# Performance work log

Hardware: AMD Instinct MI355X
Metric: run time of the kernel (lower is better)

The kernel has to match this reference:

```python
import jax, jax.numpy as jnp
import numpy as np

D_MODEL = 512
N_HEADS = 8
DH = D_MODEL // N_HEADS            # 64
Q_PROJ = D_MODEL // 2              # 256
KV_PROJ = (2 * D_MODEL) // 3       # 341
ROPE_DIM = D_MODEL // 8            # 64 total rope dims
R = ROPE_DIM // N_HEADS            # 8 rope dims per head
THETA = 10000.0
EPS = 1e-5
B, S = 2, 2048


def layernorm(x, g, b):
    m = jnp.mean(x, axis=-1, keepdims=True)
    v = jnp.var(x, axis=-1, keepdims=True)
    return (x - m) * jax.lax.rsqrt(v + EPS) * g + b


def rope_cos_sin(seq_len, dtype):
    inv_freq = THETA ** (-jnp.arange(0, R, 2, dtype=jnp.float32) / R)   # (R/2,)
    ang = jnp.arange(seq_len, dtype=jnp.float32)[:, None] * inv_freq   # (S, R/2)
    cos = jnp.concatenate([jnp.cos(ang), jnp.cos(ang)], axis=-1)        # (S, R)
    sin = jnp.concatenate([jnp.sin(ang), jnp.sin(ang)], axis=-1)
    return cos.astype(dtype), sin.astype(dtype)


def apply_rope(x, cos, sin):
    # x: (B, H, S, R); neox-style half rotation
    x1, x2 = jnp.split(x, 2, axis=-1)
    rot = jnp.concatenate([-x2, x1], axis=-1)
    return x * cos + rot * sin


def setup_inputs() -> dict:
    key = jax.random.key(0)
    ks = jax.random.split(key, 9)
    p = lambda k, shape: 0.01 * jax.random.normal(k, shape, jnp.float32)
    return {
        "x": jax.random.normal(ks[0], (B, S, D_MODEL), jnp.float32),
        "W_dq": p(ks[1], (D_MODEL, Q_PROJ)),
        "W_uq": p(ks[2], (Q_PROJ, D_MODEL)),
        "W_qr": p(ks[3], (Q_PROJ, ROPE_DIM)),
        "W_dkv": p(ks[4], (D_MODEL, KV_PROJ)),
        "W_ukv": p(ks[5], (KV_PROJ, 2 * D_MODEL)),
        "W_kr": p(ks[6], (D_MODEL, ROPE_DIM)),
        "W_o": p(ks[7], (D_MODEL, D_MODEL)),
        "q_ln_g": jnp.ones((Q_PROJ,), jnp.float32),
        "q_ln_b": jnp.zeros((Q_PROJ,), jnp.float32),
        "kv_ln_g": jnp.ones((KV_PROJ,), jnp.float32),
        "kv_ln_b": jnp.zeros((KV_PROJ,), jnp.float32),
    }


def reference(x, W_dq, W_uq, W_qr, W_dkv, W_ukv, W_kr, W_o,
              q_ln_g, q_ln_b, kv_ln_g, kv_ln_b):
    b, s, d = x.shape
    # --- low-rank Q path ---
    cq = layernorm(x @ W_dq, q_ln_g, q_ln_b)                      # (B,S,Q_PROJ)
    Q = (cq @ W_uq).reshape(b, s, N_HEADS, DH).transpose(0, 2, 1, 3)
    Qr = (cq @ W_qr).reshape(b, s, N_HEADS, R).transpose(0, 2, 1, 3)
    cos, sin = rope_cos_sin(s, x.dtype)
    Qr = apply_rope(Qr, cos, sin)
    q = jnp.concatenate([Q, Qr], axis=-1)                          # (B,H,S,DH+R)
    # --- low-rank KV path ---
    ckv = layernorm(x @ W_dkv, kv_ln_g, kv_ln_b)                  # (B,S,KV_PROJ)
    KV = ckv @ W_ukv                                              # (B,S,2*D)
    K, V = KV[..., :D_MODEL], KV[..., D_MODEL:]
    K = K.reshape(b, s, N_HEADS, DH).transpose(0, 2, 1, 3)
    Kr = (x @ W_kr).reshape(b, s, N_HEADS, R).transpose(0, 2, 1, 3)
    Kr = apply_rope(Kr, cos, sin)
    k = jnp.concatenate([K, Kr], axis=-1)                          # (B,H,S,DH+R)
    v = V.reshape(b, s, N_HEADS, DH).transpose(0, 2, 1, 3)         # (B,H,S,DH)
    # --- causal SDPA ---
    scale = 1.0 / jnp.sqrt(jnp.asarray(DH + R, x.dtype))
    scores = jnp.einsum('bhqd,bhkd->bhqk', q, k) * scale           # (B,H,S,S)
    mask = jnp.tril(jnp.ones((s, s), dtype=bool))
    scores = jnp.where(mask, scores, jnp.finfo(scores.dtype).min)
    attn = jax.nn.softmax(scores, axis=-1)
    out = jnp.einsum('bhqk,bhkd->bhqd', attn, v)
    out = out.transpose(0, 2, 1, 3).reshape(b, s, d)
    return out @ W_o.T, ckv
```

## Files before the change

### kernel.cpp

```cpp
#include <hip/hip_runtime.h>
#include <hip/hip_bf16.h>

#define BATCH 2
#define SEQ 2048
#define DM 512
#define NH 8
#define DHD 64
#define QP 256
#define KVP 341
#define DQKPAD 96
#define MROWS 4096

#define OFF_X     0
#define OFF_WO    2932224
#define OFF_QG    3194368
#define OFF_QB    3194624
#define OFF_KG    3194880
#define OFF_KB    3195221

#define T_DQ   0
#define T_DKV  131072
#define T_KR   327680
#define T_UQ   360448
#define T_QR   491520
#define T_UKV  507904
#define T_TOT  901120

#define NW_X   2097152
#define NW_WO  262144
#define NW_PAR 1194
#define PREP_TOT (NW_X + NW_WO + NW_PAR + T_TOT)

typedef __bf16 bf16x8 __attribute__((ext_vector_type(8)));
typedef float f32x4 __attribute__((ext_vector_type(4)));
typedef __hip_bfloat16 bf16;
typedef unsigned short u16;

static __device__ __forceinline__ bf16x8 ld_bf8(const bf16* p) {
    return __builtin_bit_cast(bf16x8, *(const uint4*)p);
}

#define GL16(gp, lp) __builtin_amdgcn_global_load_lds( \
    (const __attribute__((address_space(1))) void*)(gp), \
    (__attribute__((address_space(3))) void*)(lp), 16, 0, 0)

__global__ __launch_bounds__(256) void prep(
    const void* px, const void* pwdq, const void* pwuq, const void* pwqr,
    const void* pwdkv, const void* pwukv, const void* pwkr, const void* pwo,
    const void* pqg, const void* pqb, const void* pkg, const void* pkb,
    u16* __restrict__ arena, u16* __restrict__ WT, int* __restrict__ flagp)
{
    __shared__ int cnt;
    if (threadIdx.x == 0) cnt = 0;
    __syncthreads();
    int bad = 0;
    const u16* xs = (const u16*)px;
    for (int i = threadIdx.x; i < 2048; i += 256) {
        u16 u = xs[i];
        int e = (u >> 7) & 0xFF;
        if (u != 0 && (e < 90 || e > 164)) bad++;
    }
    #pragma unroll
    for (int m2 = 1; m2 < 64; m2 <<= 1) bad += __shfl_xor(bad, m2);
    if ((threadIdx.x & 63) == 0) atomicAdd(&cnt, bad);
    __syncthreads();
    const int f = (cnt > 256) ? 1 : 0;
    if (blockIdx.x == 0 && threadIdx.x == 0) *flagp = f;

    int gid = blockIdx.x * 256 + threadIdx.x;
    if (gid >= PREP_TOT) return;

    auto rdu = [&](const void* s, int i) -> u16 {
        if (f) return __builtin_bit_cast(u16, __float2bfloat16(((const float*)s)[i]));
        return ((const u16*)s)[i];
    };

    if (gid < NW_X) {
        arena[OFF_X + gid] = rdu(px, gid);
    } else if (gid < NW_X + NW_WO) {
        int i = gid - NW_X;
        arena[OFF_WO + i] = rdu(pwo, i);
    } else if (gid < NW_X + NW_WO + NW_PAR) {
        int i = gid - NW_X - NW_WO;
        if (i < 256)      arena[OFF_QG + i]         = rdu(pqg, i);
        else if (i < 512) arena[OFF_QB + (i - 256)] = rdu(pqb, i - 256);
        else if (i < 853) arena[OFF_KG + (i - 512)] = rdu(pkg, i - 512);
        else              arena[OFF_KB + (i - 853)] = rdu(pkb, i - 853);
    } else {
        int loc = gid - (NW_X + NW_WO + NW_PAR);
        const void* src; int srcIdx, valid;
        if (loc < T_DKV)      { int l2 = loc;          int n = l2 >> 9, k = l2 & 511; src = pwdq;  valid = 1;         srcIdx = k * 256 + n; }
        else if (loc < T_KR)  { int l2 = loc - T_DKV;  int n = l2 >> 9, k = l2 & 511; src = pwdkv; valid = (n < 341); srcIdx = k * 341 + n; }
        else if (loc < T_UQ)  { int l2 = loc - T_KR;   int n = l2 >> 9, k = l2 & 511; src = pwkr;  valid = 1;         srcIdx = k * 64 + n; }
        else if (loc < T_QR)  { int l2 = loc - T_UQ;   int n = l2 >> 8, k = l2 & 255; src = pwuq;  valid = 1;         srcIdx = k * 512 + n; }
        else if (loc < T_UKV) { int l2 = loc - T_QR;   int n = l2 >> 8, k = l2 & 255; src = pwqr;  valid = 1;         srcIdx = k * 64 + n; }
        else                  { int l2 = loc - T_UKV;  int n = l2 / 384, k = l2 % 384; src = pwukv; valid = (k < 341); srcIdx = k * 1024 + n; }
        WT[loc] = valid ? rdu(src, srcIdx) : (u16)0;
    }
}

static __device__ __forceinline__ void rope_epi(
    f32x4 (&acc)[2][4], bf16* __restrict__ dst, int m0, int w, int g, int lr, int tid, bool scaleq)
{
    const float SCv = 0.11785113019775793f;
    #pragma unroll
    for (int mt = 0; mt < 2; ++mt)
    #pragma unroll
    for (int r = 0; r < 4; ++r) {
        int gm = m0 + w * 32 + mt * 16 + g * 4 + r;
        int s = gm & 2047, b = gm >> 11;
        float ang = (float)s * exp2f(-(float)(lr & 3) * 3.3219280948873623f);
        float sn, cs;
        sincosf(ang, &sn, &cs);
        #pragma unroll
        for (int nt = 0; nt < 4; ++nt) {
            float v = acc[mt][nt][r];
            float pt = __shfl_xor(v, 4);
            float o = (lr & 4) ? fmaf(pt, sn, v * cs) : fmaf(-pt, sn, v * cs);
            if (scaleq) o *= SCv;
            int h = (nt * 16 + lr) >> 3, j = lr & 7;
            dst[((size_t)(b * NH + h) * SEQ + s) * DQKPAD + 64 + j] = __float2bfloat16(o);
        }
    }
    for (int u = tid; u < 128 * 96; u += 256) {
        int rw = u / 96, rem = u - rw * 96;
        int h = rem / 12, c = rem - h * 12;
        int row = m0 + rw, b2 = row >> 11, s2 = row & 2047;
        *(unsigned int*)&dst[((size_t)(b2 * NH + h) * SEQ + s2) * DQKPAD + 72 + c * 2] = 0u;
    }
}

__global__ __launch_bounds__(256) void gemm128(
    const bf16* __restrict__ A, int lda,
    const bf16* __restrict__ BT, int ldb,
    int N, int Kpad, int mode,
    void* __restrict__ C0, int ldc,
    bf16* __restrict__ kv_k, bf16* __restrict__ kv_v,
    const int* __restrict__ flagp, float* __restrict__ C0f)
{
    __shared__ __align__(16) bf16 LB[128 * 64 + 64 * 64];
    bf16* Al = LB;
    bf16* Bl = LB + 128 * 64;
    const int tid = threadIdx.x;
    const int m0 = blockIdx.y * 128, n0 = blockIdx.x * 64;
    const int lane = tid & 63, w = tid >> 6;
    const int g = lane >> 4, lr = lane & 15;
    f32x4 acc[2][4] = {};
    const int r8 = lane >> 3;
    const int xr8 = ((lane & 7) ^ r8) * 8;
    const int swx = (lr & 7) << 4;

    for (int k0 = 0; k0 < Kpad; k0 += 64) {
        #pragma unroll
        for (int i = 0; i < 4; ++i)
            GL16(&A[(size_t)(m0 + w * 32 + i * 8 + r8) * lda + k0 + xr8],
                 (char*)Al + w * 4096 + i * 1024);
        #pragma unroll
        for (int i = 0; i < 2; ++i)
            GL16(&BT[(size_t)(n0 + w * 16 + i * 8 + r8) * ldb + k0 + xr8],
                 (char*)Bl + w * 2048 + i * 1024);
        __syncthreads();
        #pragma unroll
        for (int ks = 0; ks < 2; ++ks) {
            const int cs = (ks * 64 + g * 16) ^ swx;
            bf16x8 a0 = ld_bf8((const bf16*)((const char*)Al + (w * 32 + lr) * 128 + cs));
            bf16x8 a1 = ld_bf8((const bf16*)((const char*)Al + (w * 32 + 16 + lr) * 128 + cs));
            #pragma unroll
            for (int nt = 0; nt < 4; ++nt) {
                bf16x8 b = ld_bf8((const bf16*)((const char*)Bl + (nt * 16 + lr) * 128 + cs));
                acc[0][nt] = __builtin_amdgcn_mfma_f32_16x16x32_bf16(a0, b, acc[0][nt], 0, 0, 0);
                acc[1][nt] = __builtin_amdgcn_mfma_f32_16x16x32_bf16(a1, b, acc[1][nt], 0, 0, 0);
            }
        }
        __syncthreads();
    }

    if (mode == 0 && n0 == 640) {
        rope_epi(acc, kv_k, m0, w, g, lr, tid, false);
        return;
    }
    if (mode == 4 && n0 == DM) {
        rope_epi(acc, (bf16*)C0, m0, w, g, lr, tid, true);
        return;
    }
    if (mode == 3 && n0 >= DM) {
        const int h = (n0 - DM) >> 6;
        const int b = m0 >> 11, s0 = m0 & 2047;
        bf16* T = LB;
        #pragma unroll
        for (int mt = 0; mt < 2; ++mt)
        #pragma unroll
        for (int nt = 0; nt < 4; ++nt)
        #pragma unroll
        for (int r = 0; r < 4; ++r) {
            int dv = nt * 16 + lr;
            int sl = w * 32 + mt * 16 + g * 4 + r;
            T[dv * 136 + sl] = __float2bfloat16(acc[mt][nt][r]);
        }
        __syncthreads();
        const int row = tid >> 2, coff = (tid & 3) * 32;
        bf16* dst = &kv_v[((size_t)(b * NH + h) * DHD + row) * SEQ + s0 + coff];
        const bf16* srcp = &T[row * 136 + coff];
        #pragma unroll
        for (int q2 = 0; q2 < 4; ++q2)
            *(uint4*)(dst + q2 * 8) = *(const uint4*)(srcp + q2 * 8);
        return;
    }

    const float SCv = 0.11785113019775793f;
    const int f32o = (mode == 1 && flagp) ? *flagp : 0;
    #pragma unroll
    for (int mt = 0; mt < 2; ++mt)
    #pragma unroll
    for (int nt = 0; nt < 4; ++nt)
    #pragma unroll
    for (int r = 0; r < 4; ++r) {
        int gm = m0 + w * 32 + mt * 16 + g * 4 + r;
        int gn = n0 + nt * 16 + lr;
        float v = acc[mt][nt][r];
        if (mode == 0) {
            ((float*)C0)[(size_t)gm * ldc + gn] = v;
        } else if (mode == 1) {
            if (f32o) C0f[(size_t)gm * ldc + gn] = v;
            else ((bf16*)C0)[(size_t)gm * ldc + gn] = __float2bfloat16(v);
        } else if (mode == 4) {
            int b = gm >> 11, s = gm & 2047;
            int h = gn >> 6, dh = gn & 63;
            ((bf16*)C0)[((size_t)(b * NH + h) * SEQ + s) * DQKPAD + dh] = __float2bfloat16(v * SCv);
        } else {
            int b = gm >> 11, s = gm & 2047;
            int h = gn >> 6, dh = gn & 63;
            kv_k[((size_t)(b * NH + h) * SEQ + s) * DQKPAD + dh] = __float2bfloat16(v);
        }
    }
}

__global__ __launch_bounds__(256) void ln_both(
    const float* __restrict__ y,
    const bf16* __restrict__ qg, const bf16* __restrict__ qb,
    const bf16* __restrict__ kg, const bf16* __restrict__ kb,
    bf16* __restrict__ cq, bf16* __restrict__ ckv_b, float* __restrict__ ckv_f,
    bf16* __restrict__ ckvp, const int* __restrict__ flagp)
{
    const int w = threadIdx.x >> 6, lane = threadIdx.x & 63;
    const int blk = blockIdx.x;
    if (blk < 1024) {
        const int row = blk * 4 + w;
        const float* yr = y + (size_t)row * 704;
        float s = 0.f, ss = 0.f;
        for (int i = lane; i < 256; i += 64) { float v = yr[i]; s += v; ss += v * v; }
        #pragma unroll
        for (int m = 1; m < 64; m <<= 1) { s += __shfl_xor(s, m); ss += __shfl_xor(ss, m); }
        float mean = s * (1.f / 256.f);
        float var = ss * (1.f / 256.f) - mean * mean;
        float rstd = rsqrtf(var + 1e-5f);
        for (int i = lane; i < 256; i += 64) {
            float v = (yr[i] - mean) * rstd * __bfloat162float(qg[i]) + __bfloat162float(qb[i]);
            cq[(size_t)row * 256 + i] = __float2bfloat16(v);
        }
    } else {
        const int row = (blk - 1024) * 4 + w;
        const float* yr = y + (size_t)row * 704 + 256;
        const int f32o = *flagp;
        float s = 0.f, ss = 0.f;
        for (int i = lane; i < KVP; i += 64) { float v = yr[i]; s += v; ss += v * v; }
        #pragma unroll
        for (int m = 1; m < 64; m <<= 1) { s += __shfl_xor(s, m); ss += __shfl_xor(ss, m); }
        float mean = s * (1.f / 341.f);
        float var = ss * (1.f / 341.f) - mean * mean;
        float rstd = rsqrtf(var + 1e-5f);
        for (int i = lane; i < KVP; i += 64) {
            float v = (yr[i] - mean) * rstd * __bfloat162float(kg[i]) + __bfloat162float(kb[i]);
            if (f32o) ckv_f[(size_t)row * KVP + i] = v;
            else ckv_b[(size_t)row * KVP + i] = __float2bfloat16(v);
            ckvp[(size_t)row * 384 + i] = __float2bfloat16(v);
        }
        for (int i = KVP + lane; i < 384; i += 64) ckvp[(size_t)row * 384 + i] = __float2bfloat16(0.f);
    }
}

__global__ __launch_bounds__(256) void attn_split3(
    const bf16* __restrict__ qa, const bf16* __restrict__ ka, const bf16* __restrict__ vat,
    bf16* __restrict__ po, float* __restrict__ mlm, float* __restrict__ mll)
{
    __shared__ __align__(16) bf16 Kl[64][104];
    __shared__ __align__(16) bf16 Vt[64][72];
    __shared__ __align__(16) bf16 Pl[4][16][72];
    const int sp = blockIdx.x, pr = blockIdx.y, bh = blockIdx.z;
    const int tid = threadIdx.x, w = tid >> 6, lane = tid & 63;
    const int g = lane >> 4, lr = lane & 15;
    const size_t base = (size_t)bh * SEQ;
    const float L2E = 1.4426950408889634f;
    const bf16* vb = vat + (size_t)bh * DHD * SEQ;

    for (int half = 0; half < 2; ++half) {
        const int qb = half ? (31 - pr) : pr;
        const int qrow0 = qb * 64 + w * 16;
        const int myq = qrow0 + lr;

        bf16x8 qf[3];
        #pragma unroll
        for (int kc = 0; kc < 3; ++kc)
            qf[kc] = ld_bf8(&qa[(base + myq) * DQKPAD + kc * 32 + g * 8]);

        float m_p = -1e30f, l_p = 0.f;
        f32x4 acc_o[4] = {};
        const int ng = qb + 1;
        const int bs = (ng * sp) >> 2, be = (ng * (sp + 1)) >> 2;

        for (int gi = bs; gi < be; ++gi) {
            const int j0 = gi * 64;
            __syncthreads();
            for (int u = tid; u < 768; u += 256) {
                int row = u / 12, cc = (u % 12) * 8;
                *(uint4*)&Kl[row][cc] = *(const uint4*)&ka[(base + j0 + row) * DQKPAD + cc];
            }
            {
                int d = tid >> 2, ko = (tid & 3) * 16;
                const bf16* vsrc = &vb[(size_t)d * SEQ + j0 + ko];
                *(uint4*)&Vt[d][ko]     = *(const uint4*)vsrc;
                *(uint4*)&Vt[d][ko + 8] = *(const uint4*)(vsrc + 8);
            }
            __syncthreads();

            f32x4 accs[4] = {};
            #pragma unroll
            for (int kc = 0; kc < 3; ++kc) {
                #pragma unroll
                for (int nt = 0; nt < 4; ++nt) {
                    bf16x8 kf = ld_bf8(&Kl[nt * 16 + lr][kc * 32 + g * 8]);
                    accs[nt] = __builtin_amdgcn_mfma_f32_16x16x32_bf16(kf, qf[kc], accs[nt], 0, 0, 0);
                }
            }
            float s_[4][4];
            float mloc = -1e30f;
            if (j0 + 63 > qrow0) {
                #pragma unroll
                for (int nt = 0; nt < 4; ++nt)
                #pragma unroll
                for (int r = 0; r < 4; ++r) {
                    int key = j0 + nt * 16 + g * 4 + r;
                    float sv = accs[nt][r];
                    sv = (key <= myq) ? sv : -1e30f;
                    s_[nt][r] = sv;
                    mloc = fmaxf(mloc, sv);
                }
            } else {
                #pragma unroll
                for (int nt = 0; nt < 4; ++nt)
                #pragma unroll
                for (int r = 0; r < 4; ++r) {
                    float sv = accs[nt][r];
                    s_[nt][r] = sv;
                    mloc = fmaxf(mloc, sv);
                }
            }
            mloc = fmaxf(mloc, __shfl_xor(mloc, 16));
            mloc = fmaxf(mloc, __shfl_xor(mloc, 32));

            if (__all(mloc <= m_p + 8.f)) {
                float rs = 0.f;
                #pragma unroll
                for (int nt = 0; nt < 4; ++nt)
                #pragma unroll
                for (int r = 0; r < 4; ++r) {
                    float p = exp2f((s_[nt][r] - m_p) * L2E);
                    s_[nt][r] = p; rs += p;
                }
                rs += __shfl_xor(rs, 16);
                rs += __shfl_xor(rs, 32);
                l_p += rs;
            } else {
                float mn = fmaxf(m_p, mloc);
                float alpha = exp2f((m_p - mn) * L2E);
                m_p = mn;
                float rs = 0.f;
                #pragma unroll
                for (int nt = 0; nt < 4; ++nt)
                #pragma unroll
                for (int r = 0; r < 4; ++r) {
                    float p = exp2f((s_[nt][r] - mn) * L2E);
                    s_[nt][r] = p; rs += p;
                }
                rs += __shfl_xor(rs, 16);
                rs += __shfl_xor(rs, 32);
                l_p = l_p * alpha + rs;
                float ar[4];
                #pragma unroll
                for (int r = 0; r < 4; ++r) ar[r] = __shfl(alpha, g * 4 + r);
                #pragma unroll
                for (int nv = 0; nv < 4; ++nv)
                #pragma unroll
                for (int r = 0; r < 4; ++r) acc_o[nv][r] *= ar[r];
            }
            #pragma unroll
            for (int nt = 0; nt < 4; ++nt) {
                ushort4 pk;
                pk.x = __builtin_bit_cast(u16, __float2bfloat16(s_[nt][0]));
                pk.y = __builtin_bit_cast(u16, __float2bfloat16(s_[nt][1]));
                pk.z = __builtin_bit_cast(u16, __float2bfloat16(s_[nt][2]));
                pk.w = __builtin_bit_cast(u16, __float2bfloat16(s_[nt][3]));
                *(ushort4*)&Pl[w][lr][nt * 16 + g * 4] = pk;
            }
            bf16x8 pf0 = ld_bf8(&Pl[w][lr][g * 8]);
            bf16x8 pf1 = ld_bf8(&Pl[w][lr][32 + g * 8]);
            #pragma unroll
            for (int nv = 0; nv < 4; ++nv) {
                bf16x8 vf0 = ld_bf8(&Vt[nv * 16 + lr][g * 8]);
                acc_o[nv] = __builtin_amdgcn_mfma_f32_16x16x32_bf16(pf0, vf0, acc_o[nv], 0, 0, 0);
                bf16x8 vf1 = ld_bf8(&Vt[nv * 16 + lr][32 + g * 8]);
                acc_o[nv] = __builtin_amdgcn_mfma_f32_16x16x32_bf16(pf1, vf1, acc_o[nv], 0, 0, 0);
            }
        }

        const size_t pb = (size_t)(bh * 4 + sp) * SEQ;
        #pragma unroll
        for (int r = 0; r < 4; ++r) {
            int qrow = qrow0 + g * 4 + r;
            #pragma unroll
            for (int nv = 0; nv < 4; ++nv)
                po[(pb + qrow) * DHD + nv * 16 + lr] = __float2bfloat16(acc_o[nv][r]);
        }
        if (lane < 16) {
            mlm[pb + qrow0 + lane] = m_p;
            mll[pb + qrow0 + lane] = l_p;
        }
    }
}

__global__ __launch_bounds__(256) void attn_combine(
    const bf16* __restrict__ po, const float* __restrict__ mlm, const float* __restrict__ mll,
    bf16* __restrict__ ao)
{
    int id = blockIdx.x * 256 + threadIdx.x;
    int bh = id >> 14;
    int rem = id & 16383;
    int q = rem >> 3, dc = (rem & 7) * 8;
    const float L2E = 1.4426950408889634f;
    size_t mlb = (size_t)bh * 4 * SEQ + q;
    float ms[4], ls[4];
    #pragma unroll
    for (int s = 0; s < 4; ++s) { ms[s] = mlm[mlb + (size_t)s * SEQ]; ls[s] = mll[mlb + (size_t)s * SEQ]; }
    float M = fmaxf(fmaxf(ms[0], ms[1]), fmaxf(ms[2], ms[3]));
    float wsc[4]; float L = 0.f;
    #pragma unroll
    for (int s = 0; s < 4; ++s) { wsc[s] = exp2f((ms[s] - M) * L2E); L += wsc[s] * ls[s]; }
    float o[8] = {};
    #pragma unroll
    for (int s = 0; s < 4; ++s) {
        if (ls[s] <= 0.f) continue;
        bf16x8 pv = ld_bf8(&po[((size_t)(bh * 4 + s) * SEQ + q) * DHD + dc]);
        #pragma unroll
        for (int j = 0; j < 8; ++j) o[j] += wsc[s] * (float)pv[j];
    }
    float invL = 1.f / L;
    int b = bh >> 3, h = bh & 7;
    __bf16 tmp[8];
    #pragma unroll
    for (int j = 0; j < 8; ++j) tmp[j] = (__bf16)(o[j] * invL);
    *(uint4*)&ao[((size_t)(b * SEQ) + q) * DM + h * DHD + dc] = *(uint4*)tmp;
}

extern "C" void kernel_launch(void* const* d_in, const int* in_sizes, int n_in,
                              void* d_out, int out_size, void* d_ws, size_t ws_size,
                              hipStream_t stream) {
    char* ws = (char*)d_ws;
    bf16* AR      = (bf16*)(ws + 0);
    float* ml_m   = (float*)(ws + 0);
    float* ml_l   = (float*)(ws + 524288);
    bf16* WT      = (bf16*)(ws + 6391296);
    int*  flagp   = (int*)(ws + 8193536);
    float* y      = (float*)(ws + 8194048);
    bf16* cq      = (bf16*)(ws + 19728384);
    bf16* ckvp    = (bf16*)(ws + 21825536);
    bf16* po      = (bf16*)(ws + 8194048);
    bf16* q_attn  = (bf16*)(ws + 26019840);
    bf16* k_attn  = (bf16*)(ws + 32311296);
    bf16* v_attnT = (bf16*)(ws + 38602752);
    bf16* attn_o  = (bf16*)(ws + 42797056);

    const bf16* xb  = AR + OFF_X;
    const bf16* W_o = AR + OFF_WO;
    const bf16* qg  = AR + OFF_QG;
    const bf16* qb_ = AR + OFF_QB;
    const bf16* kg  = AR + OFF_KG;
    const bf16* kb  = AR + OFF_KB;

    bf16*  out_b = (bf16*)d_out;
    float* out_f = (float*)d_out;
    bf16*  ckv_b = out_b + (size_t)MROWS * DM;
    float* ckv_f = out_f + (size_t)MROWS * DM;

    dim3 blk(256);
    prep<<<dim3((PREP_TOT + 255) / 256), blk, 0, stream>>>(
        d_in[0], d_in[1], d_in[2], d_in[3], d_in[4], d_in[5],
        d_in[6], d_in[7], d_in[8], d_in[9], d_in[10], d_in[11],
        (u16*)AR, (u16*)WT, flagp);
    gemm128<<<dim3(11, 32), blk, 0, stream>>>(xb, DM, WT + T_DQ, DM, 704, DM, 0, y, 704, k_attn, nullptr, nullptr, nullptr);
    ln_both<<<dim3(2048), blk, 0, stream>>>(y, qg, qb_, kg, kb, cq, ckv_b, ckv_f, ckvp, flagp);
    gemm128<<<dim3(9, 32), blk, 0, stream>>>(cq, QP, WT + T_UQ, QP, 576, QP, 4, q_attn, 0, nullptr, nullptr, nullptr, nullptr);
    gemm128<<<dim3(16, 32), blk, 0, stream>>>(ckvp, 384, WT + T_UKV, 384, 1024, 384, 3, nullptr, 0, k_attn, v_attnT, nullptr, nullptr);
    attn_split3<<<dim3(4, 16, 16), blk, 0, stream>>>(q_attn, k_attn, v_attnT, po, ml_m, ml_l);
    attn_combine<<<dim3(1024), blk, 0, stream>>>(po, ml_m, ml_l, attn_o);
    gemm128<<<dim3(8, 32), blk, 0, stream>>>(attn_o, DM, W_o, DM, DM, DM, 1, out_b, DM, nullptr, nullptr, flagp, out_f);
}
```

Measured before the change: 127.9 us.

## Vectorize prep conversion and raise attention key-split count to eight

The prep kernel now has each thread handle 8 contiguous elements, with 16-byte loads and stores for x and W_o and packed 8-wide writes for the transposed weights. This cuts the thread count and the per-element indexing cost. Attention splits the key range into 8 partitions instead of 4, giving twice as many blocks for the causal workload. The combine kernel now merges 8 partial results, so partial-output memory and combine traffic grow; the partial buffers move to a new workspace offset to make room.

```diff
diff --git a/kernel.cpp b/kernel.cpp
--- a/kernel.cpp
+++ b/kernel.cpp
@@ -29,7 +29,14 @@
 #define NW_X   2097152
 #define NW_WO  262144
 #define NW_PAR 1194
-#define PREP_TOT (NW_X + NW_WO + NW_PAR + T_TOT)
+
+#define G_X   262144
+#define G_WO  32768
+#define G_PAR 150
+#define G_WT  112640
+#define G_TOT (G_X + G_WO + G_PAR + G_WT)
+
+#define NSPLIT 8
 
 typedef __bf16 bf16x8 __attribute__((ext_vector_type(8)));
 typedef float f32x4 __attribute__((ext_vector_type(4)));
@@ -68,34 +75,52 @@
     if (blockIdx.x == 0 && threadIdx.x == 0) *flagp = f;
 
     int gid = blockIdx.x * 256 + threadIdx.x;
-    if (gid >= PREP_TOT) return;
+    if (gid >= G_TOT) return;
 
     auto rdu = [&](const void* s, int i) -> u16 {
         if (f) return __builtin_bit_cast(u16, __float2bfloat16(((const float*)s)[i]));
         return ((const u16*)s)[i];
     };
 
-    if (gid < NW_X) {
-        arena[OFF_X + gid] = rdu(px, gid);
-    } else if (gid < NW_X + NW_WO) {
-        int i = gid - NW_X;
-        arena[OFF_WO + i] = rdu(pwo, i);
-    } else if (gid < NW_X + NW_WO + NW_PAR) {
-        int i = gid - NW_X - NW_WO;
-        if (i < 256)      arena[OFF_QG + i]         = rdu(pqg, i);
-        else if (i < 512) arena[OFF_QB + (i - 256)] = rdu(pqb, i - 256);
-        else if (i < 853) arena[OFF_KG + (i - 512)] = rdu(pkg, i - 512);
-        else              arena[OFF_KB + (i - 853)] = rdu(pkb, i - 853);
+    if (gid < G_X + G_WO) {
+        const void* src = (gid < G_X) ? px : pwo;
+        int base = (gid < G_X) ? OFF_X : OFF_WO;
+        int i = (gid < G_X) ? gid : gid - G_X;
+        u16 out[8];
+        if (f) {
+            const float* s = (const float*)src + i * 8;
+            #pragma unroll
+            for (int j = 0; j < 8; ++j) out[j] = __builtin_bit_cast(u16, __float2bfloat16(s[j]));
+        } else {
+            *(uint4*)out = ((const uint4*)src)[i];
+        }
+        *(uint4*)&arena[base + i * 8] = *(uint4*)out;
+    } else if (gid < G_X + G_WO + G_PAR) {
+        int i0 = (gid - G_X - G_WO) * 8;
+        for (int j = 0; j < 8; ++j) {
+            int i = i0 + j;
+            if (i >= NW_PAR) break;
+            if (i < 256)      arena[OFF_QG + i]         = rdu(pqg, i);
+            else if (i < 512) arena[OFF_QB + (i - 256)] = rdu(pqb, i - 256);
+            else if (i < 853) arena[OFF_KG + (i - 512)] = rdu(pkg, i - 512);
+            else              arena[OFF_KB + (i - 853)] = rdu(pkb, i - 853);
+        }
     } else {
-        int loc = gid - (NW_X + NW_WO + NW_PAR);
-        const void* src; int srcIdx, valid;
-        if (loc < T_DKV)      { int l2 = loc;          int n = l2 >> 9, k = l2 & 511; src = pwdq;  valid = 1;         srcIdx = k * 256 + n; }
-        else if (loc < T_KR)  { int l2 = loc - T_DKV;  int n = l2 >> 9, k = l2 & 511; src = pwdkv; valid = (n < 341); srcIdx = k * 341 + n; }
-        else if (loc < T_UQ)  { int l2 = loc - T_KR;   int n = l2 >> 9, k = l2 & 511; src = pwkr;  valid = 1;         srcIdx = k * 64 + n; }
-        else if (loc < T_QR)  { int l2 = loc - T_UQ;   int n = l2 >> 8, k = l2 & 255; src = pwuq;  valid = 1;         srcIdx = k * 512 + n; }
-        else if (loc < T_UKV) { int l2 = loc - T_QR;   int n = l2 >> 8, k = l2 & 255; src = pwqr;  valid = 1;         srcIdx = k * 64 + n; }
-        else                  { int l2 = loc - T_UKV;  int n = l2 / 384, k = l2 % 384; src = pwukv; valid = (k < 341); srcIdx = k * 1024 + n; }
-        WT[loc] = valid ? rdu(src, srcIdx) : (u16)0;
+        int loc = (gid - (G_X + G_WO + G_PAR)) * 8;
+        const void* src; int n, k0, sN, klim, nok;
+        if (loc < T_DKV)      { int l = loc;          n = l >> 9; k0 = l & 511; src = pwdq;  sN = 256;  klim = 512; nok = 1; }
+        else if (loc < T_KR)  { int l = loc - T_DKV;  n = l >> 9; k0 = l & 511; src = pwdkv; sN = 341;  klim = 512; nok = (n < 341); }
+        else if (loc < T_UQ)  { int l = loc - T_KR;   n = l >> 9; k0 = l & 511; src = pwkr;  sN = 64;   klim = 512; nok = 1; }
+        else if (loc < T_QR)  { int l = loc - T_UQ;   n = l >> 8; k0 = l & 255; src = pwuq;  sN = 512;  klim = 256; nok = 1; }
+        else if (loc < T_UKV) { int l = loc - T_QR;   n = l >> 8; k0 = l & 255; src = pwqr;  sN = 64;   klim = 256; nok = 1; }
+        else                  { int l = loc - T_UKV;  n = l / 384; k0 = l % 384; src = pwukv; sN = 1024; klim = 341; nok = 1; }
+        u16 out[8];
+        #pragma unroll
+        for (int j = 0; j < 8; ++j) {
+            int k = k0 + j;
+            out[j] = (nok && k < klim) ? rdu(src, k * sN + n) : (u16)0;
+        }
+        *(uint4*)&WT[loc] = *(uint4*)out;
     }
 }
 
@@ -306,7 +331,7 @@
         float m_p = -1e30f, l_p = 0.f;
         f32x4 acc_o[4] = {};
         const int ng = qb + 1;
-        const int bs = (ng * sp) >> 2, be = (ng * (sp + 1)) >> 2;
+        const int bs = (ng * sp) >> 3, be = (ng * (sp + 1)) >> 3;
 
         for (int gi = bs; gi < be; ++gi) {
             const int j0 = gi * 64;
@@ -413,7 +438,7 @@
             }
         }
 
-        const size_t pb = (size_t)(bh * 4 + sp) * SEQ;
+        const size_t pb = (size_t)(bh * NSPLIT + sp) * SEQ;
         #pragma unroll
         for (int r = 0; r < 4; ++r) {
             int qrow = qrow0 + g * 4 + r;
@@ -437,19 +462,21 @@
     int rem = id & 16383;
     int q = rem >> 3, dc = (rem & 7) * 8;
     const float L2E = 1.4426950408889634f;
-    size_t mlb = (size_t)bh * 4 * SEQ + q;
-    float ms[4], ls[4];
-    #pragma unroll
-    for (int s = 0; s < 4; ++s) { ms[s] = mlm[mlb + (size_t)s * SEQ]; ls[s] = mll[mlb + (size_t)s * SEQ]; }
-    float M = fmaxf(fmaxf(ms[0], ms[1]), fmaxf(ms[2], ms[3]));
-    float wsc[4]; float L = 0.f;
-    #pragma unroll
-    for (int s = 0; s < 4; ++s) { wsc[s] = exp2f((ms[s] - M) * L2E); L += wsc[s] * ls[s]; }
+    size_t mlb = (size_t)bh * NSPLIT * SEQ + q;
+    float ms[NSPLIT], ls[NSPLIT];
+    #pragma unroll
+    for (int s = 0; s < NSPLIT; ++s) { ms[s] = mlm[mlb + (size_t)s * SEQ]; ls[s] = mll[mlb + (size_t)s * SEQ]; }
+    float M = -1e30f;
+    #pragma unroll
+    for (int s = 0; s < NSPLIT; ++s) M = fmaxf(M, ms[s]);
+    float wsc[NSPLIT]; float L = 0.f;
+    #pragma unroll
+    for (int s = 0; s < NSPLIT; ++s) { wsc[s] = exp2f((ms[s] - M) * L2E); L += wsc[s] * ls[s]; }
     float o[8] = {};
     #pragma unroll
-    for (int s = 0; s < 4; ++s) {
+    for (int s = 0; s < NSPLIT; ++s) {
         if (ls[s] <= 0.f) continue;
-        bf16x8 pv = ld_bf8(&po[((size_t)(bh * 4 + s) * SEQ + q) * DHD + dc]);
+        bf16x8 pv = ld_bf8(&po[((size_t)(bh * NSPLIT + s) * SEQ + q) * DHD + dc]);
         #pragma unroll
         for (int j = 0; j < 8; ++j) o[j] += wsc[s] * (float)pv[j];
     }
@@ -467,17 +494,17 @@
     char* ws = (char*)d_ws;
     bf16* AR      = (bf16*)(ws + 0);
     float* ml_m   = (float*)(ws + 0);
-    float* ml_l   = (float*)(ws + 524288);
+    float* ml_l   = (float*)(ws + 1048576);
     bf16* WT      = (bf16*)(ws + 6391296);
     int*  flagp   = (int*)(ws + 8193536);
     float* y      = (float*)(ws + 8194048);
     bf16* cq      = (bf16*)(ws + 19728384);
     bf16* ckvp    = (bf16*)(ws + 21825536);
-    bf16* po      = (bf16*)(ws + 8194048);
     bf16* q_attn  = (bf16*)(ws + 26019840);
     bf16* k_attn  = (bf16*)(ws + 32311296);
     bf16* v_attnT = (bf16*)(ws + 38602752);
     bf16* attn_o  = (bf16*)(ws + 42797056);
+    bf16* po      = (bf16*)(ws + 50331648);
 
     const bf16* xb  = AR + OFF_X;
     const bf16* W_o = AR + OFF_WO;
@@ -492,7 +519,7 @@
     float* ckv_f = out_f + (size_t)MROWS * DM;
 
     dim3 blk(256);
-    prep<<<dim3((PREP_TOT + 255) / 256), blk, 0, stream>>>(
+    prep<<<dim3((G_TOT + 255) / 256), blk, 0, stream>>>(
         d_in[0], d_in[1], d_in[2], d_in[3], d_in[4], d_in[5],
         d_in[6], d_in[7], d_in[8], d_in[9], d_in[10], d_in[11],
         (u16*)AR, (u16*)WT, flagp);
@@ -500,7 +527,7 @@
     ln_both<<<dim3(2048), blk, 0, stream>>>(y, qg, qb_, kg, kb, cq, ckv_b, ckv_f, ckvp, flagp);
     gemm128<<<dim3(9, 32), blk, 0, stream>>>(cq, QP, WT + T_UQ, QP, 576, QP, 4, q_attn, 0, nullptr, nullptr, nullptr, nullptr);
     gemm128<<<dim3(16, 32), blk, 0, stream>>>(ckvp, 384, WT + T_UKV, 384, 1024, 384, 3, nullptr, 0, k_attn, v_attnT, nullptr, nullptr);
-    attn_split3<<<dim3(4, 16, 16), blk, 0, stream>>>(q_attn, k_attn, v_attnT, po, ml_m, ml_l);
+    attn_split3<<<dim3(NSPLIT, 16, 16), blk, 0, stream>>>(q_attn, k_attn, v_attnT, po, ml_m, ml_l);
     attn_combine<<<dim3(1024), blk, 0, stream>>>(po, ml_m, ml_l, attn_o);
     gemm128<<<dim3(8, 32), blk, 0, stream>>>(attn_o, DM, W_o, DM, DM, DM, 1, out_b, DM, nullptr, nullptr, flagp, out_f);
 }
```

Result: no change. 126.3 us (-1.2%).
